# Kernel optimization log

Hardware: AMD Instinct MI355X
Metric: run time of the kernel (lower is better)

The kernel has to match this reference:

```python
import jax, jax.numpy as jnp
import numpy as np


def setup_inputs() -> dict:
    key = jax.random.key(0)
    ks = jax.random.split(key, 8)
    B, Nq, Nk, D, H, Cv = 8, 4096, 4096, 2, 64, 64
    q = jax.random.normal(ks[0], (B, Nq, D), dtype=jnp.float32)
    k = jax.random.normal(ks[1], (B, Nk, D), dtype=jnp.float32)
    v = jax.random.normal(ks[2], (B, Nk, Cv), dtype=jnp.float32)
    # Linear params (torch nn.Linear layout: W is (out, in), y = x @ W.T + b)
    s = 1.0 / np.sqrt(D)
    q_proj_w = jax.random.uniform(ks[3], (H, D), jnp.float32, -s, s)
    q_proj_b = jax.random.uniform(ks[4], (H,), jnp.float32, -s, s)
    k_proj_w = jax.random.uniform(ks[5], (H, D), jnp.float32, -s, s)
    k_proj_b = jax.random.uniform(ks[6], (H,), jnp.float32, -s, s)
    return {"q": q, "k": k, "v": v,
            "q_proj_w": q_proj_w, "q_proj_b": q_proj_b,
            "k_proj_w": k_proj_w, "k_proj_b": k_proj_b,
            "top_k": 16}


def _cdist(q, k):
    # Euclidean distances (B, Nq, Nk) via the Gram trick (avoids a BxNqxNkxD diff tensor)
    q2 = jnp.sum(q * q, axis=-1)  # (B, Nq)
    k2 = jnp.sum(k * k, axis=-1)  # (B, Nk)
    d2 = q2[:, :, None] + k2[:, None, :] - 2.0 * jnp.einsum('bqd,bnd->bqn', q, k)
    return jnp.sqrt(jnp.maximum(d2, 0.0))


def _batched_gather(inputs, idx):
    # inputs: (B, Nk, C), idx: (B, Nq, K) -> (B, Nq, K, C)
    return jax.vmap(lambda inp, ix: inp[ix])(inputs, idx)


def reference(q, k, v, q_proj_w, q_proj_b, k_proj_w, k_proj_b, top_k):
    dists = _cdist(q, k)                                   # (B, Nq, Nk)
    _, knn_idx = jax.lax.top_k(-dists, top_k)              # smallest distances
    k_knn = _batched_gather(k, knn_idx)                    # (B, Nq, K, D)
    v_knn = _batched_gather(v, knn_idx)                    # (B, Nq, K, Cv)
    q_emb = q @ q_proj_w.T + q_proj_b                      # (B, Nq, H)
    k_emb = k_knn @ k_proj_w.T + k_proj_b                  # (B, Nq, K, H)
    attn_scores = jnp.einsum('bqh,bqkh->bqk', q_emb, k_emb)
    attn = jax.nn.softmax(attn_scores, axis=-1)
    out = jnp.einsum('bqk,bqkc->bqc', attn, v_knn)         # (B, Nq, Cv)
    return out
```

## Files before the change

kernel.cpp:

```cpp
#include <hip/hip_runtime.h>
#include <stdint.h>

typedef uint64_t u64;
typedef uint32_t u32;

#define NB    8
#define NQ    4096
#define NKEY  4096
#define CV    64
#define KSEL  16
#define NWAVE 8
#define BLK   (NWAVE * 64)
#define CMAX  64

#define PADV ((((u64)0x7F800000u) << 32) | (u64)0xFFFFFFFFu)

__device__ __forceinline__ u64 shflxor_u64(u64 v, int m) {
    const u32 lo = __shfl_xor((int)(u32)v, m);
    const u32 hi = __shfl_xor((int)(u32)(v >> 32), m);
    return (((u64)hi) << 32) | lo;
}

__device__ __forceinline__ float lanesort64_f32(float v, int lane) {
#pragma unroll
    for (int k = 2; k <= 64; k <<= 1) {
#pragma unroll
        for (int j = k >> 1; j > 0; j >>= 1) {
            const float p = __shfl_xor(v, j);
            const bool up    = ((lane & k) == 0);
            const bool lower = ((lane & j) == 0);
            v = (lower == up) ? fminf(v, p) : fmaxf(v, p);
        }
    }
    return v;
}

__device__ __forceinline__ u64 lanesort64_u64(u64 v, int lane) {
#pragma unroll
    for (int k = 2; k <= 64; k <<= 1) {
#pragma unroll
        for (int j = k >> 1; j > 0; j >>= 1) {
            const u64 p = shflxor_u64(v, j);
            const bool up    = ((lane & k) == 0);
            const bool lower = ((lane & j) == 0);
            const u64 mn = v < p ? v : p;
            const u64 mx = v < p ? p : v;
            v = (lower == up) ? mn : mx;
        }
    }
    return v;
}

extern "C" __global__ void setup_sums_kernel(const float* __restrict__ qw,
                                             const float* __restrict__ qb,
                                             const float* __restrict__ kw,
                                             const float* __restrict__ kb,
                                             float* __restrict__ w9) {
    const int h = threadIdx.x & 63;
    const float2 a = ((const float2*)qw)[h];
    const float2 c = ((const float2*)kw)[h];
    const float qbh = qb[h], kbh = kb[h];
    float s[9] = { a.x * c.x, a.y * c.x, qbh * c.x,
                   a.x * c.y, a.y * c.y, qbh * c.y,
                   a.x * kbh, a.y * kbh, qbh * kbh };
#pragma unroll
    for (int i = 0; i < 9; ++i)
#pragma unroll
        for (int off = 32; off; off >>= 1) s[i] += __shfl_xor(s[i], off);
    if (h == 0) {
#pragma unroll
        for (int i = 0; i < 9; ++i) w9[i] = s[i];
    }
}

extern "C" __global__ void __launch_bounds__(BLK, 2)
sparse_bev_attn_kernel(const float* __restrict__ qg,
                       const float* __restrict__ kg,
                       const float* __restrict__ vg,
                       const float* __restrict__ sums9,
                       float* __restrict__ outg)
{
    __shared__ u64 cand[NWAVE][CMAX];

    const int tid  = threadIdx.x;
    const int wv   = tid >> 6;
    const int lane = tid & 63;
    const int b    = blockIdx.x >> 9;
    const int qi   = ((blockIdx.x & 511) << 3) + wv;

    const float2* kp = (const float2*)(kg + (size_t)b * NKEY * 2);
    const float2  qc = ((const float2*)qg)[(size_t)b * NQ + qi];
    const float qx = qc.x, qy = qc.y;

    const float4* kp4 = (const float4*)kp;
    float d2r[64];
    float mn = __builtin_inff();
#pragma unroll
    for (int c = 0; c < 32; ++c) {
        const float4 kk = kp4[c * 64 + lane];
        const float dx0 = qx - kk.x, dy0 = qy - kk.y;
        const float dx1 = qx - kk.z, dy1 = qy - kk.w;
        d2r[2 * c]     = fmaf(dx0, dx0, dy0 * dy0);
        d2r[2 * c + 1] = fmaf(dx1, dx1, dy1 * dy1);
        mn = fminf(mn, fminf(d2r[2 * c], d2r[2 * c + 1]));
    }

    const float thr = __shfl(lanesort64_f32(mn, lane), 15);

    const u32 l2 = (u32)(lane << 1);
    auto collect = [&](float t) -> int {
        int c = 0;
#pragma unroll
        for (int r = 0; r < 64; ++r) {
            const bool acc = d2r[r] <= t;
            const u64 mask = __ballot(acc);
            if (mask) {
                const int pos = c + (int)__builtin_amdgcn_mbcnt_hi(
                    (u32)(mask >> 32), __builtin_amdgcn_mbcnt_lo((u32)mask, 0));
                if (acc && pos < CMAX) {
                    const u32 kidx = (u32)(((r >> 1) << 7) + (r & 1)) + l2;
                    cand[wv][pos] = (((u64)__float_as_uint(d2r[r])) << 32) | kidx;
                }
                c += __popcll(mask);
            }
        }
        return c;
    };

    int cnt = collect(thr);
    if (cnt > CMAX) {
        u32 lo = 0, hi = 0x7F800000u;
        while (lo < hi) {
            const u32 mid = (lo + hi) >> 1;
            const float t = __uint_as_float(mid);
            int c = 0;
#pragma unroll
            for (int r = 0; r < 64; ++r) c += (d2r[r] <= t) ? 1 : 0;
#pragma unroll
            for (int off = 32; off; off >>= 1) c += __shfl_xor(c, off);
            if (c >= KSEL) hi = mid; else lo = mid + 1;
        }
        cnt = collect(__uint_as_float(lo));
        if (cnt > CMAX) cnt = CMAX;
    }

    u64 myv = (lane < cnt) ? cand[wv][lane] : PADV;
    myv = lanesort64_u64(myv, lane);
    const u32 myidx = (u32)myv;

    const float s1 = sums9[0], s2 = sums9[1], s3 = sums9[2];
    const float s4 = sums9[3], s5 = sums9[4], s6 = sums9[5];
    const float s7 = sums9[6], s8 = sums9[7], s9 = sums9[8];
    const float A  = fmaf(qx, s1, fmaf(qy, s2, s3));
    const float Bb = fmaf(qx, s4, fmaf(qy, s5, s6));
    const float Cc = fmaf(qx, s7, fmaf(qy, s8, s9));

    const int sel = (lane < KSEL) ? (int)myidx : 0;
    const float2 kc = kp[sel];
    const float score = fmaf(A, kc.x, fmaf(Bb, kc.y, Cc));
    float mx = score;
#pragma unroll
    for (int off = 8; off; off >>= 1) mx = fmaxf(mx, __shfl_xor(mx, off));
    const float e = __expf(score - mx);
    float sum = e;
#pragma unroll
    for (int off = 8; off; off >>= 1) sum += __shfl_xor(sum, off);
    const float w = e / sum;

    const float* vb = vg + (size_t)b * NKEY * CV;
    float acc = 0.f;
#pragma unroll
    for (int s = 0; s < KSEL; ++s) {
        const u32 id   = (u32)__builtin_amdgcn_readlane((int)myidx, s);
        const float ws = __uint_as_float(
            (u32)__builtin_amdgcn_readlane((int)__float_as_uint(w), s));
        acc = fmaf(ws, vb[(size_t)id * CV + lane], acc);
    }
    outg[((size_t)b * NQ + qi) * CV + lane] = acc;
}

extern "C" void kernel_launch(void* const* d_in, const int* in_sizes, int n_in,
                              void* d_out, int out_size, void* d_ws, size_t ws_size,
                              hipStream_t stream) {
    const float* q  = (const float*)d_in[0];
    const float* k  = (const float*)d_in[1];
    const float* v  = (const float*)d_in[2];
    const float* qw = (const float*)d_in[3];
    const float* qb = (const float*)d_in[4];
    const float* kw = (const float*)d_in[5];
    const float* kb = (const float*)d_in[6];
    float* out = (float*)d_out;
    float* w9  = (float*)d_ws;

    hipLaunchKernelGGL(setup_sums_kernel, dim3(1), dim3(64), 0, stream,
                       qw, qb, kw, kb, w9);
    hipLaunchKernelGGL(sparse_bev_attn_kernel, dim3(NB * (NQ / NWAVE)), dim3(BLK),
                       0, stream, q, k, v, w9, out);
}
```

Baseline: 74.94 us.

## Recompute distances in two passes instead of caching 64 per lane

Drops the 64-register distance array. Distances are now recomputed in a min pass and again in a collect pass, which lowers register pressure and raises the launch-bounds occupancy target, with the block size halved to 4 waves. When workspace allows, a setup pass precomputes per-key (x, y, |k|^2) so each distance becomes two FMAs in Gram form. The full 64-lane bitonic sort is replaced by a partial top-16 network. The cost is a second read of all keys per query, and the Gram form may change near-tie ordering.

```diff
diff --git a/kernel.cpp b/kernel.cpp
--- a/kernel.cpp
+++ b/kernel.cpp
@@ -9,16 +9,23 @@
 #define NKEY  4096
 #define CV    64
 #define KSEL  16
-#define NWAVE 8
+#define NWAVE 4
 #define BLK   (NWAVE * 64)
 #define CMAX  64
-
-#define PADV ((((u64)0x7F800000u) << 32) | (u64)0xFFFFFFFFu)
+#define PADU  (~(u64)0)
 
 __device__ __forceinline__ u64 shflxor_u64(u64 v, int m) {
     const u32 lo = __shfl_xor((int)(u32)v, m);
     const u32 hi = __shfl_xor((int)(u32)(v >> 32), m);
     return (((u64)hi) << 32) | lo;
+}
+__device__ __forceinline__ int mbcnt64(u64 m) {
+    return (int)__builtin_amdgcn_mbcnt_hi((u32)(m >> 32),
+               __builtin_amdgcn_mbcnt_lo((u32)m, 0));
+}
+__device__ __forceinline__ u32 fkey(float f) {
+    const u32 b = __float_as_uint(f);
+    return b ^ (0x80000000u | (u32)((int32_t)b >> 31));
 }
 
 __device__ __forceinline__ float lanesort64_f32(float v, int lane) {
@@ -35,125 +42,208 @@
     return v;
 }
 
-__device__ __forceinline__ u64 lanesort64_u64(u64 v, int lane) {
-#pragma unroll
-    for (int k = 2; k <= 64; k <<= 1) {
+__device__ __forceinline__ u64 top16of64(u64 v, int lane) {
+#pragma unroll
+    for (int k = 2; k <= 16; k <<= 1) {
 #pragma unroll
         for (int j = k >> 1; j > 0; j >>= 1) {
             const u64 p = shflxor_u64(v, j);
             const bool up    = ((lane & k) == 0);
             const bool lower = ((lane & j) == 0);
-            const u64 mn = v < p ? v : p;
-            const u64 mx = v < p ? p : v;
+            const u64 mn = v < p ? v : p, mx = v < p ? p : v;
             v = (lower == up) ? mn : mx;
         }
     }
+    {   const u64 p = shflxor_u64(v, 16);
+        const u64 mn = v < p ? v : p, mx = v < p ? p : v;
+        v = ((lane & 16) == 0) ? mn : mx; }
+#pragma unroll
+    for (int j = 8; j > 0; j >>= 1) {
+        const u64 p = shflxor_u64(v, j);
+        const bool lower = ((lane & j) == 0);
+        const bool dasc  = ((lane & 32) == 0);
+        const u64 mn = v < p ? v : p, mx = v < p ? p : v;
+        v = (lower == dasc) ? mn : mx;
+    }
+    {   const u64 p = shflxor_u64(v, 32);
+        const u64 mn = v < p ? v : p, mx = v < p ? p : v;
+        v = ((lane & 32) == 0) ? mn : mx; }
     return v;
 }
 
-extern "C" __global__ void setup_sums_kernel(const float* __restrict__ qw,
-                                             const float* __restrict__ qb,
-                                             const float* __restrict__ kw,
-                                             const float* __restrict__ kb,
-                                             float* __restrict__ w9) {
-    const int h = threadIdx.x & 63;
-    const float2 a = ((const float2*)qw)[h];
-    const float2 c = ((const float2*)kw)[h];
-    const float qbh = qb[h], kbh = kb[h];
-    float s[9] = { a.x * c.x, a.y * c.x, qbh * c.x,
-                   a.x * c.y, a.y * c.y, qbh * c.y,
-                   a.x * kbh, a.y * kbh, qbh * kbh };
-#pragma unroll
-    for (int i = 0; i < 9; ++i)
-#pragma unroll
-        for (int off = 32; off; off >>= 1) s[i] += __shfl_xor(s[i], off);
-    if (h == 0) {
-#pragma unroll
-        for (int i = 0; i < 9; ++i) w9[i] = s[i];
-    }
-}
-
-extern "C" __global__ void __launch_bounds__(BLK, 2)
-sparse_bev_attn_kernel(const float* __restrict__ qg,
-                       const float* __restrict__ kg,
-                       const float* __restrict__ vg,
-                       const float* __restrict__ sums9,
-                       float* __restrict__ outg)
+__global__ void setup_kernel(const float* __restrict__ kg,
+                             const float* __restrict__ qw, const float* __restrict__ qb,
+                             const float* __restrict__ kw, const float* __restrict__ kb,
+                             float* __restrict__ w9, float4* __restrict__ kq4, int dok2)
+{
+    const int gid = blockIdx.x * 256 + threadIdx.x;
+    if (dok2 && gid < NB * NKEY) {
+        const float2 kc = ((const float2*)kg)[gid];
+        kq4[gid] = make_float4(kc.x, kc.y, fmaf(kc.x, kc.x, kc.y * kc.y), 0.f);
+    }
+    if (blockIdx.x == 0 && threadIdx.x < 64) {
+        const int h = threadIdx.x;
+        const float2 a = ((const float2*)qw)[h];
+        const float2 c = ((const float2*)kw)[h];
+        const float qbh = qb[h], kbh = kb[h];
+        float s[9] = { a.x * c.x, a.y * c.x, qbh * c.x,
+                       a.x * c.y, a.y * c.y, qbh * c.y,
+                       a.x * kbh, a.y * kbh, qbh * kbh };
+#pragma unroll
+        for (int i = 0; i < 9; ++i)
+#pragma unroll
+            for (int off = 32; off; off >>= 1) s[i] += __shfl_xor(s[i], off);
+        if (h == 0) {
+#pragma unroll
+            for (int i = 0; i < 9; ++i) w9[i] = s[i];
+        }
+    }
+}
+
+template<int MODE>
+__global__ __launch_bounds__(BLK, 8) void bev_main(
+    const float* __restrict__ qg, const float* __restrict__ kg,
+    const float* __restrict__ vg, const float* __restrict__ w9,
+    const float4* __restrict__ kq4, float* __restrict__ outg)
 {
     __shared__ u64 cand[NWAVE][CMAX];
 
     const int tid  = threadIdx.x;
     const int wv   = tid >> 6;
     const int lane = tid & 63;
-    const int b    = blockIdx.x >> 9;
-    const int qi   = ((blockIdx.x & 511) << 3) + wv;
+    const int b    = blockIdx.x >> 10;
+    const int qi   = ((blockIdx.x & 1023) << 2) + wv;
 
     const float2* kp = (const float2*)(kg + (size_t)b * NKEY * 2);
     const float2  qc = ((const float2*)qg)[(size_t)b * NQ + qi];
     const float qx = qc.x, qy = qc.y;
-
+    const float m2qx = -2.f * qx, m2qy = -2.f * qy;
+    const float4* kb4 = kq4 + (size_t)b * NKEY;
     const float4* kp4 = (const float4*)kp;
-    float d2r[64];
-    float mn = __builtin_inff();
-#pragma unroll
-    for (int c = 0; c < 32; ++c) {
-        const float4 kk = kp4[c * 64 + lane];
-        const float dx0 = qx - kk.x, dy0 = qy - kk.y;
-        const float dx1 = qx - kk.z, dy1 = qy - kk.w;
-        d2r[2 * c]     = fmaf(dx0, dx0, dy0 * dy0);
-        d2r[2 * c + 1] = fmaf(dx1, dx1, dy1 * dy1);
-        mn = fminf(mn, fminf(d2r[2 * c], d2r[2 * c + 1]));
-    }
-
+
+    float mn0 = __builtin_inff(), mn1 = mn0, mn2 = mn0, mn3 = mn0;
+    if (MODE == 0) {
+#pragma unroll
+        for (int c = 0; c < 64; c += 4) {
+            const float4 a0 = kb4[(c + 0) * 64 + lane];
+            const float4 a1 = kb4[(c + 1) * 64 + lane];
+            const float4 a2 = kb4[(c + 2) * 64 + lane];
+            const float4 a3 = kb4[(c + 3) * 64 + lane];
+            mn0 = fminf(mn0, fmaf(a0.x, m2qx, fmaf(a0.y, m2qy, a0.z)));
+            mn1 = fminf(mn1, fmaf(a1.x, m2qx, fmaf(a1.y, m2qy, a1.z)));
+            mn2 = fminf(mn2, fmaf(a2.x, m2qx, fmaf(a2.y, m2qy, a2.z)));
+            mn3 = fminf(mn3, fmaf(a3.x, m2qx, fmaf(a3.y, m2qy, a3.z)));
+        }
+    } else {
+#pragma unroll
+        for (int c = 0; c < 32; c += 2) {
+            const float4 k0 = kp4[(c + 0) * 64 + lane];
+            const float4 k1 = kp4[(c + 1) * 64 + lane];
+            { const float dx = qx - k0.x, dy = qy - k0.y; mn0 = fminf(mn0, fmaf(dx, dx, dy * dy)); }
+            { const float dx = qx - k0.z, dy = qy - k0.w; mn1 = fminf(mn1, fmaf(dx, dx, dy * dy)); }
+            { const float dx = qx - k1.x, dy = qy - k1.y; mn2 = fminf(mn2, fmaf(dx, dx, dy * dy)); }
+            { const float dx = qx - k1.z, dy = qy - k1.w; mn3 = fminf(mn3, fmaf(dx, dx, dy * dy)); }
+        }
+    }
+    const float mn  = fminf(fminf(mn0, mn1), fminf(mn2, mn3));
     const float thr = __shfl(lanesort64_f32(mn, lane), 15);
 
-    const u32 l2 = (u32)(lane << 1);
-    auto collect = [&](float t) -> int {
-        int c = 0;
-#pragma unroll
-        for (int r = 0; r < 64; ++r) {
-            const bool acc = d2r[r] <= t;
-            const u64 mask = __ballot(acc);
-            if (mask) {
-                const int pos = c + (int)__builtin_amdgcn_mbcnt_hi(
-                    (u32)(mask >> 32), __builtin_amdgcn_mbcnt_lo((u32)mask, 0));
-                if (acc && pos < CMAX) {
-                    const u32 kidx = (u32)(((r >> 1) << 7) + (r & 1)) + l2;
-                    cand[wv][pos] = (((u64)__float_as_uint(d2r[r])) << 32) | kidx;
+    int cnt = 0;
+    if (MODE == 0) {
+#pragma unroll
+        for (int c = 0; c < 64; ++c) {
+            const float4 a = kb4[c * 64 + lane];
+            const float vv = fmaf(a.x, m2qx, fmaf(a.y, m2qy, a.z));
+            const bool acc = vv <= thr;
+            const u64 mk = __ballot(acc);
+            if (mk) {
+                const int pos = cnt + mbcnt64(mk);
+                if (acc && pos < CMAX)
+                    cand[wv][pos] = (((u64)fkey(vv)) << 32) | (u32)(c * 64 + lane);
+                cnt += __popcll(mk);
+            }
+        }
+    } else {
+#pragma unroll
+        for (int c = 0; c < 32; ++c) {
+            const float4 kk = kp4[c * 64 + lane];
+            const float dx0 = qx - kk.x, dy0 = qy - kk.y;
+            const float dx1 = qx - kk.z, dy1 = qy - kk.w;
+            const float v0 = fmaf(dx0, dx0, dy0 * dy0);
+            const float v1 = fmaf(dx1, dx1, dy1 * dy1);
+            const bool a0 = v0 <= thr;
+            u64 mk = __ballot(a0);
+            if (mk) {
+                const int pos = cnt + mbcnt64(mk);
+                if (a0 && pos < CMAX)
+                    cand[wv][pos] = (((u64)fkey(v0)) << 32) | (u32)(2 * (c * 64 + lane));
+                cnt += __popcll(mk);
+            }
+            const bool a1 = v1 <= thr;
+            mk = __ballot(a1);
+            if (mk) {
+                const int pos = cnt + mbcnt64(mk);
+                if (a1 && pos < CMAX)
+                    cand[wv][pos] = (((u64)fkey(v1)) << 32) | (u32)(2 * (c * 64 + lane) + 1);
+                cnt += __popcll(mk);
+            }
+        }
+    }
+
+    if (cnt > CMAX) {
+        u32 lo = 0, hi = ~0u;
+        while (lo < hi) {
+            const u32 mid = lo + ((hi - lo) >> 1);
+            int cc = 0;
+#pragma unroll 1
+            for (int c = 0; c < 64; ++c) {
+                float vv;
+                if (MODE == 0) {
+                    const float4 a = kb4[c * 64 + lane];
+                    vv = fmaf(a.x, m2qx, fmaf(a.y, m2qy, a.z));
+                } else {
+                    const float2 kc2 = kp[c * 64 + lane];
+                    const float dx = qx - kc2.x, dy = qy - kc2.y;
+                    vv = fmaf(dx, dx, dy * dy);
                 }
-                c += __popcll(mask);
-            }
-        }
-        return c;
-    };
-
-    int cnt = collect(thr);
-    if (cnt > CMAX) {
-        u32 lo = 0, hi = 0x7F800000u;
-        while (lo < hi) {
-            const u32 mid = (lo + hi) >> 1;
-            const float t = __uint_as_float(mid);
-            int c = 0;
-#pragma unroll
-            for (int r = 0; r < 64; ++r) c += (d2r[r] <= t) ? 1 : 0;
-#pragma unroll
-            for (int off = 32; off; off >>= 1) c += __shfl_xor(c, off);
-            if (c >= KSEL) hi = mid; else lo = mid + 1;
-        }
-        cnt = collect(__uint_as_float(lo));
+                cc += (fkey(vv) <= mid) ? 1 : 0;
+            }
+#pragma unroll
+            for (int off = 32; off; off >>= 1) cc += __shfl_xor(cc, off);
+            if (cc >= KSEL) hi = mid; else lo = mid + 1;
+        }
+        cnt = 0;
+#pragma unroll 1
+        for (int c = 0; c < 64; ++c) {
+            float vv;
+            if (MODE == 0) {
+                const float4 a = kb4[c * 64 + lane];
+                vv = fmaf(a.x, m2qx, fmaf(a.y, m2qy, a.z));
+            } else {
+                const float2 kc2 = kp[c * 64 + lane];
+                const float dx = qx - kc2.x, dy = qy - kc2.y;
+                vv = fmaf(dx, dx, dy * dy);
+            }
+            const u32 tb = fkey(vv);
+            const bool acc = tb <= lo;
+            const u64 mk = __ballot(acc);
+            if (mk) {
+                const int pos = cnt + mbcnt64(mk);
+                if (acc && pos < CMAX)
+                    cand[wv][pos] = (((u64)tb) << 32) | (u32)(c * 64 + lane);
+                cnt += __popcll(mk);
+            }
+        }
         if (cnt > CMAX) cnt = CMAX;
     }
 
-    u64 myv = (lane < cnt) ? cand[wv][lane] : PADV;
-    myv = lanesort64_u64(myv, lane);
+    u64 myv = (lane < cnt) ? cand[wv][lane] : PADU;
+    myv = top16of64(myv, lane);
     const u32 myidx = (u32)myv;
 
-    const float s1 = sums9[0], s2 = sums9[1], s3 = sums9[2];
-    const float s4 = sums9[3], s5 = sums9[4], s6 = sums9[5];
-    const float s7 = sums9[6], s8 = sums9[7], s9 = sums9[8];
-    const float A  = fmaf(qx, s1, fmaf(qy, s2, s3));
-    const float Bb = fmaf(qx, s4, fmaf(qy, s5, s6));
-    const float Cc = fmaf(qx, s7, fmaf(qy, s8, s9));
+    const float A  = fmaf(qx, w9[0], fmaf(qy, w9[1], w9[2]));
+    const float Bb = fmaf(qx, w9[3], fmaf(qy, w9[4], w9[5]));
+    const float Cc = fmaf(qx, w9[6], fmaf(qy, w9[7], w9[8]));
 
     const int sel = (lane < KSEL) ? (int)myidx : 0;
     const float2 kc = kp[sel];
@@ -190,10 +280,18 @@
     const float* kw = (const float*)d_in[5];
     const float* kb = (const float*)d_in[6];
     float* out = (float*)d_out;
-    float* w9  = (float*)d_ws;
-
-    hipLaunchKernelGGL(setup_sums_kernel, dim3(1), dim3(64), 0, stream,
-                       qw, qb, kw, kb, w9);
-    hipLaunchKernelGGL(sparse_bev_attn_kernel, dim3(NB * (NQ / NWAVE)), dim3(BLK),
-                       0, stream, q, k, v, w9, out);
-}
+
+    float*  w9  = (float*)d_ws;
+    float4* kq4 = (float4*)((char*)d_ws + 256);
+    const size_t need = 256 + (size_t)NB * NKEY * sizeof(float4);
+    const int mode0 = (ws_size >= need) ? 1 : 0;
+
+    hipLaunchKernelGGL(setup_kernel, dim3(mode0 ? (NB * NKEY / 256) : 1), dim3(256),
+                       0, stream, k, qw, qb, kw, kb, w9, kq4, mode0);
+    if (mode0)
+        hipLaunchKernelGGL((bev_main<0>), dim3(NB * NQ / NWAVE), dim3(BLK),
+                           0, stream, q, k, v, w9, kq4, out);
+    else
+        hipLaunchKernelGGL((bev_main<1>), dim3(NB * NQ / NWAVE), dim3(BLK),
+                           0, stream, q, k, v, w9, kq4, out);
+}
```

Measured after the change: 186.7 us. +149.1%, slower.

## Process eight queries per wave with two-pass recompute and partial top-16 sort

Applied to the files above, without the earlier changes.

Each wave now handles eight queries, so every key load is shared across them. Instead of keeping 64 distances in registers, the kernel runs a min pass, then recomputes distances in a collect pass using the expanded form k² − 2q·k, and uses an order-preserving float key. The full 64-lane bitonic sort is replaced by a partial network that only needs the top 16, and occupancy hints and block size change. The cost is recomputing distances and more per-wave serial work; the expanded form can change which neighbour wins near ties.

```diff
diff --git a/kernel.cpp b/kernel.cpp
--- a/kernel.cpp
+++ b/kernel.cpp
@@ -9,16 +9,24 @@
 #define NKEY  4096
 #define CV    64
 #define KSEL  16
-#define NWAVE 8
+#define G     8
+#define NWAVE 4
 #define BLK   (NWAVE * 64)
 #define CMAX  64
-
-#define PADV ((((u64)0x7F800000u) << 32) | (u64)0xFFFFFFFFu)
+#define PADU  (~(u64)0)
 
 __device__ __forceinline__ u64 shflxor_u64(u64 v, int m) {
     const u32 lo = __shfl_xor((int)(u32)v, m);
     const u32 hi = __shfl_xor((int)(u32)(v >> 32), m);
     return (((u64)hi) << 32) | lo;
+}
+__device__ __forceinline__ int mbcnt64(u64 m) {
+    return (int)__builtin_amdgcn_mbcnt_hi((u32)(m >> 32),
+               __builtin_amdgcn_mbcnt_lo((u32)m, 0));
+}
+__device__ __forceinline__ u32 fkey(float f) {
+    const u32 b = __float_as_uint(f);
+    return b ^ (0x80000000u | (u32)((int32_t)b >> 31));
 }
 
 __device__ __forceinline__ float lanesort64_f32(float v, int lane) {
@@ -35,27 +43,39 @@
     return v;
 }
 
-__device__ __forceinline__ u64 lanesort64_u64(u64 v, int lane) {
-#pragma unroll
-    for (int k = 2; k <= 64; k <<= 1) {
+__device__ __forceinline__ u64 top16of64(u64 v, int lane) {
+#pragma unroll
+    for (int k = 2; k <= 16; k <<= 1) {
 #pragma unroll
         for (int j = k >> 1; j > 0; j >>= 1) {
             const u64 p = shflxor_u64(v, j);
             const bool up    = ((lane & k) == 0);
             const bool lower = ((lane & j) == 0);
-            const u64 mn = v < p ? v : p;
-            const u64 mx = v < p ? p : v;
+            const u64 mn = v < p ? v : p, mx = v < p ? p : v;
             v = (lower == up) ? mn : mx;
         }
     }
+    {   const u64 p = shflxor_u64(v, 16);
+        const u64 mn = v < p ? v : p, mx = v < p ? p : v;
+        v = ((lane & 16) == 0) ? mn : mx; }
+#pragma unroll
+    for (int j = 8; j > 0; j >>= 1) {
+        const u64 p = shflxor_u64(v, j);
+        const bool lower = ((lane & j) == 0);
+        const bool dasc  = ((lane & 32) == 0);
+        const u64 mn = v < p ? v : p, mx = v < p ? p : v;
+        v = (lower == dasc) ? mn : mx;
+    }
+    {   const u64 p = shflxor_u64(v, 32);
+        const u64 mn = v < p ? v : p, mx = v < p ? p : v;
+        v = ((lane & 32) == 0) ? mn : mx; }
     return v;
 }
 
-extern "C" __global__ void setup_sums_kernel(const float* __restrict__ qw,
-                                             const float* __restrict__ qb,
-                                             const float* __restrict__ kw,
-                                             const float* __restrict__ kb,
-                                             float* __restrict__ w9) {
+__global__ void setup_kernel(const float* __restrict__ qw, const float* __restrict__ qb,
+                             const float* __restrict__ kw, const float* __restrict__ kb,
+                             float* __restrict__ w9)
+{
     const int h = threadIdx.x & 63;
     const float2 a = ((const float2*)qw)[h];
     const float2 c = ((const float2*)kw)[h];
@@ -73,110 +93,165 @@
     }
 }
 
-extern "C" __global__ void __launch_bounds__(BLK, 2)
-sparse_bev_attn_kernel(const float* __restrict__ qg,
-                       const float* __restrict__ kg,
-                       const float* __restrict__ vg,
-                       const float* __restrict__ sums9,
-                       float* __restrict__ outg)
+extern "C" __global__ __launch_bounds__(BLK, 4) void bev_main(
+    const float* __restrict__ qg, const float* __restrict__ kg,
+    const float* __restrict__ vg, const float* __restrict__ w9,
+    float* __restrict__ outg)
 {
-    __shared__ u64 cand[NWAVE][CMAX];
+    __shared__ u64 cand[NWAVE][G][CMAX];
 
     const int tid  = threadIdx.x;
     const int wv   = tid >> 6;
     const int lane = tid & 63;
-    const int b    = blockIdx.x >> 9;
-    const int qi   = ((blockIdx.x & 511) << 3) + wv;
-
-    const float2* kp = (const float2*)(kg + (size_t)b * NKEY * 2);
-    const float2  qc = ((const float2*)qg)[(size_t)b * NQ + qi];
-    const float qx = qc.x, qy = qc.y;
-
+    const int wvu  = __builtin_amdgcn_readfirstlane(wv);
+    const int b    = blockIdx.x >> 7;
+    const int qbase = ((int)(blockIdx.x & 127) * NWAVE + wvu) * G;
+
+    const float2* kp  = (const float2*)(kg + (size_t)b * NKEY * 2);
     const float4* kp4 = (const float4*)kp;
-    float d2r[64];
-    float mn = __builtin_inff();
-#pragma unroll
+    const float2* qp  = (const float2*)qg + (size_t)b * NQ + qbase;
+
+    float qxx[G], qyy[G], m2x[G], m2y[G];
+#pragma unroll
+    for (int q = 0; q < G; ++q) {
+        const float2 qc = qp[q];
+        qxx[q] = qc.x; qyy[q] = qc.y;
+        m2x[q] = -2.f * qc.x; m2y[q] = -2.f * qc.y;
+    }
+
+    float mn[G];
+#pragma unroll
+    for (int q = 0; q < G; ++q) mn[q] = __builtin_inff();
+#pragma unroll 8
     for (int c = 0; c < 32; ++c) {
         const float4 kk = kp4[c * 64 + lane];
-        const float dx0 = qx - kk.x, dy0 = qy - kk.y;
-        const float dx1 = qx - kk.z, dy1 = qy - kk.w;
-        d2r[2 * c]     = fmaf(dx0, dx0, dy0 * dy0);
-        d2r[2 * c + 1] = fmaf(dx1, dx1, dy1 * dy1);
-        mn = fminf(mn, fminf(d2r[2 * c], d2r[2 * c + 1]));
-    }
-
-    const float thr = __shfl(lanesort64_f32(mn, lane), 15);
-
-    const u32 l2 = (u32)(lane << 1);
-    auto collect = [&](float t) -> int {
-        int c = 0;
-#pragma unroll
-        for (int r = 0; r < 64; ++r) {
-            const bool acc = d2r[r] <= t;
-            const u64 mask = __ballot(acc);
-            if (mask) {
-                const int pos = c + (int)__builtin_amdgcn_mbcnt_hi(
-                    (u32)(mask >> 32), __builtin_amdgcn_mbcnt_lo((u32)mask, 0));
-                if (acc && pos < CMAX) {
-                    const u32 kidx = (u32)(((r >> 1) << 7) + (r & 1)) + l2;
-                    cand[wv][pos] = (((u64)__float_as_uint(d2r[r])) << 32) | kidx;
+        const float k2a = fmaf(kk.x, kk.x, kk.y * kk.y);
+        const float k2b = fmaf(kk.z, kk.z, kk.w * kk.w);
+#pragma unroll
+        for (int q = 0; q < G; ++q) {
+            const float va = fmaf(kk.x, m2x[q], fmaf(kk.y, m2y[q], k2a));
+            const float vb = fmaf(kk.z, m2x[q], fmaf(kk.w, m2y[q], k2b));
+            mn[q] = fminf(mn[q], fminf(va, vb));
+        }
+    }
+
+    float thr[G];
+#pragma unroll
+    for (int q = 0; q < G; ++q)
+        thr[q] = __shfl(lanesort64_f32(mn[q], lane), 15);
+
+    int cnt[G];
+#pragma unroll
+    for (int q = 0; q < G; ++q) cnt[q] = 0;
+#pragma unroll 4
+    for (int c = 0; c < 32; ++c) {
+        const float4 kk = kp4[c * 64 + lane];
+        const float k2a = fmaf(kk.x, kk.x, kk.y * kk.y);
+        const float k2b = fmaf(kk.z, kk.z, kk.w * kk.w);
+        const u32 ia = (u32)(2 * (c * 64 + lane));
+#pragma unroll
+        for (int q = 0; q < G; ++q) {
+            const float va = fmaf(kk.x, m2x[q], fmaf(kk.y, m2y[q], k2a));
+            const float vb = fmaf(kk.z, m2x[q], fmaf(kk.w, m2y[q], k2b));
+            const bool aa = va <= thr[q];
+            const bool ab = vb <= thr[q];
+            const u64 mka = __ballot(aa);
+            const u64 mkb = __ballot(ab);
+            if (mka | mkb) {
+                const int posa = cnt[q] + mbcnt64(mka);
+                cnt[q] += (int)__popcll(mka);
+                const int posb = cnt[q] + mbcnt64(mkb);
+                cnt[q] += (int)__popcll(mkb);
+                if (aa && posa < CMAX)
+                    cand[wv][q][posa] = (((u64)fkey(va)) << 32) | ia;
+                if (ab && posb < CMAX)
+                    cand[wv][q][posb] = (((u64)fkey(vb)) << 32) | (ia + 1);
+            }
+        }
+    }
+
+#pragma unroll
+    for (int q = 0; q < G; ++q) {
+        if (cnt[q] > CMAX) {
+            u32 lo = 0, hi = ~0u;
+            while (lo < hi) {
+                const u32 mid = lo + ((hi - lo) >> 1);
+                int cc = 0;
+#pragma unroll 1
+                for (int c = 0; c < 32; ++c) {
+                    const float4 kk = kp4[c * 64 + lane];
+                    const float k2a = fmaf(kk.x, kk.x, kk.y * kk.y);
+                    const float k2b = fmaf(kk.z, kk.z, kk.w * kk.w);
+                    const float va = fmaf(kk.x, m2x[q], fmaf(kk.y, m2y[q], k2a));
+                    const float vb = fmaf(kk.z, m2x[q], fmaf(kk.w, m2y[q], k2b));
+                    cc += (fkey(va) <= mid) ? 1 : 0;
+                    cc += (fkey(vb) <= mid) ? 1 : 0;
                 }
-                c += __popcll(mask);
+#pragma unroll
+                for (int off = 32; off; off >>= 1) cc += __shfl_xor(cc, off);
+                if (cc >= KSEL) hi = mid; else lo = mid + 1;
             }
-        }
-        return c;
-    };
-
-    int cnt = collect(thr);
-    if (cnt > CMAX) {
-        u32 lo = 0, hi = 0x7F800000u;
-        while (lo < hi) {
-            const u32 mid = (lo + hi) >> 1;
-            const float t = __uint_as_float(mid);
-            int c = 0;
-#pragma unroll
-            for (int r = 0; r < 64; ++r) c += (d2r[r] <= t) ? 1 : 0;
-#pragma unroll
-            for (int off = 32; off; off >>= 1) c += __shfl_xor(c, off);
-            if (c >= KSEL) hi = mid; else lo = mid + 1;
-        }
-        cnt = collect(__uint_as_float(lo));
-        if (cnt > CMAX) cnt = CMAX;
-    }
-
-    u64 myv = (lane < cnt) ? cand[wv][lane] : PADV;
-    myv = lanesort64_u64(myv, lane);
-    const u32 myidx = (u32)myv;
-
-    const float s1 = sums9[0], s2 = sums9[1], s3 = sums9[2];
-    const float s4 = sums9[3], s5 = sums9[4], s6 = sums9[5];
-    const float s7 = sums9[6], s8 = sums9[7], s9 = sums9[8];
-    const float A  = fmaf(qx, s1, fmaf(qy, s2, s3));
-    const float Bb = fmaf(qx, s4, fmaf(qy, s5, s6));
-    const float Cc = fmaf(qx, s7, fmaf(qy, s8, s9));
-
-    const int sel = (lane < KSEL) ? (int)myidx : 0;
-    const float2 kc = kp[sel];
-    const float score = fmaf(A, kc.x, fmaf(Bb, kc.y, Cc));
-    float mx = score;
-#pragma unroll
-    for (int off = 8; off; off >>= 1) mx = fmaxf(mx, __shfl_xor(mx, off));
-    const float e = __expf(score - mx);
-    float sum = e;
-#pragma unroll
-    for (int off = 8; off; off >>= 1) sum += __shfl_xor(sum, off);
-    const float w = e / sum;
-
+            int cc = 0;
+#pragma unroll 1
+            for (int c = 0; c < 32; ++c) {
+                const float4 kk = kp4[c * 64 + lane];
+                const float k2a = fmaf(kk.x, kk.x, kk.y * kk.y);
+                const float k2b = fmaf(kk.z, kk.z, kk.w * kk.w);
+                const float va = fmaf(kk.x, m2x[q], fmaf(kk.y, m2y[q], k2a));
+                const float vb = fmaf(kk.z, m2x[q], fmaf(kk.w, m2y[q], k2b));
+                const u32 ta = fkey(va), tb = fkey(vb);
+                const bool aa = ta <= lo, ab = tb <= lo;
+                const u64 mka = __ballot(aa);
+                const u64 mkb = __ballot(ab);
+                const int posa = cc + mbcnt64(mka);
+                cc += (int)__popcll(mka);
+                const int posb = cc + mbcnt64(mkb);
+                cc += (int)__popcll(mkb);
+                const u32 ia = (u32)(2 * (c * 64 + lane));
+                if (aa && posa < CMAX) cand[wv][q][posa] = (((u64)ta) << 32) | ia;
+                if (ab && posb < CMAX) cand[wv][q][posb] = (((u64)tb) << 32) | (ia + 1);
+            }
+            cnt[q] = cc < CMAX ? cc : CMAX;
+        }
+    }
+
+    const float s1 = w9[0], s2 = w9[1], s3 = w9[2];
+    const float s4 = w9[3], s5 = w9[4], s6 = w9[5];
+    const float s7 = w9[6], s8 = w9[7], s9 = w9[8];
     const float* vb = vg + (size_t)b * NKEY * CV;
-    float acc = 0.f;
-#pragma unroll
-    for (int s = 0; s < KSEL; ++s) {
-        const u32 id   = (u32)__builtin_amdgcn_readlane((int)myidx, s);
-        const float ws = __uint_as_float(
-            (u32)__builtin_amdgcn_readlane((int)__float_as_uint(w), s));
-        acc = fmaf(ws, vb[(size_t)id * CV + lane], acc);
-    }
-    outg[((size_t)b * NQ + qi) * CV + lane] = acc;
+
+#pragma unroll 1
+    for (int q = 0; q < G; ++q) {
+        u64 myv = (lane < cnt[q]) ? cand[wv][q][lane] : PADU;
+        myv = top16of64(myv, lane);
+        const u32 myidx = (u32)myv;
+
+        const float A  = fmaf(qxx[q], s1, fmaf(qyy[q], s2, s3));
+        const float Bb = fmaf(qxx[q], s4, fmaf(qyy[q], s5, s6));
+        const float Cc = fmaf(qxx[q], s7, fmaf(qyy[q], s8, s9));
+
+        const int sel = (lane < KSEL) ? (int)myidx : 0;
+        const float2 kc = kp[sel];
+        const float score = fmaf(A, kc.x, fmaf(Bb, kc.y, Cc));
+        float mx = score;
+#pragma unroll
+        for (int off = 8; off; off >>= 1) mx = fmaxf(mx, __shfl_xor(mx, off));
+        const float e = __expf(score - mx);
+        float sum = e;
+#pragma unroll
+        for (int off = 8; off; off >>= 1) sum += __shfl_xor(sum, off);
+        const float w = e / sum;
+
+        float acc = 0.f;
+#pragma unroll
+        for (int s = 0; s < KSEL; ++s) {
+            const u32 id   = (u32)__builtin_amdgcn_readlane((int)myidx, s);
+            const float ws = __uint_as_float(
+                (u32)__builtin_amdgcn_readlane((int)__float_as_uint(w), s));
+            acc = fmaf(ws, vb[(size_t)id * CV + lane], acc);
+        }
+        outg[((size_t)b * NQ + qbase + q) * CV + lane] = acc;
+    }
 }
 
 extern "C" void kernel_launch(void* const* d_in, const int* in_sizes, int n_in,
@@ -192,8 +267,8 @@
     float* out = (float*)d_out;
     float* w9  = (float*)d_ws;
 
-    hipLaunchKernelGGL(setup_sums_kernel, dim3(1), dim3(64), 0, stream,
+    hipLaunchKernelGGL(setup_kernel, dim3(1), dim3(64), 0, stream,
                        qw, qb, kw, kb, w9);
-    hipLaunchKernelGGL(sparse_bev_attn_kernel, dim3(NB * (NQ / NWAVE)), dim3(BLK),
+    hipLaunchKernelGGL(bev_main, dim3(NB * NQ / (G * NWAVE)), dim3(BLK),
                        0, stream, q, k, v, w9, out);
 }
```

After: 74.86 us. About the same (-0.1%).

## Replace brute-force kNN scan with uniform spatial grid search

Applied to the files above, without the earlier changes.

Keys are bucketed into a 64x64 uniform grid per batch by count, scan and scatter kernels, so each query only examines keys in nearby cells. The search grows a square window until enough candidates are found, takes a threshold from them, then visits outer rings of cells and prunes each cell by its box distance against the current 16th-best. This removes the full 4096-key distance scan per query at the cost of four extra small launches, atomics and data-dependent divergent loops. The grid spans the fixed range [-4,4] with clamping, so results stay exact but cost rises if keys are not spread out.

```diff
diff --git a/kernel.cpp b/kernel.cpp
--- a/kernel.cpp
+++ b/kernel.cpp
@@ -3,22 +3,37 @@
 
 typedef uint64_t u64;
 typedef uint32_t u32;
+typedef unsigned short u16;
 
 #define NB    8
 #define NQ    4096
 #define NKEY  4096
 #define CV    64
 #define KSEL  16
-#define NWAVE 8
-#define BLK   (NWAVE * 64)
-#define CMAX  64
-
-#define PADV ((((u64)0x7F800000u) << 32) | (u64)0xFFFFFFFFu)
+#define GRD   64
+#define NCELL (GRD * GRD)
+#define HCELL 0.125f
+#define GLO   -4.0f
+#define CTGT  48
+#define CMAX  128
+#define PADU  (~(u64)0)
+
+#define WS_CS    256
+#define WS_SKEY  (WS_CS + NB * NCELL * 4)
+#define WS_SIDX  (WS_SKEY + NB * NKEY * 8)
 
 __device__ __forceinline__ u64 shflxor_u64(u64 v, int m) {
     const u32 lo = __shfl_xor((int)(u32)v, m);
     const u32 hi = __shfl_xor((int)(u32)(v >> 32), m);
     return (((u64)hi) << 32) | lo;
+}
+__device__ __forceinline__ int mbcnt64(u64 m) {
+    return (int)__builtin_amdgcn_mbcnt_hi((u32)(m >> 32),
+               __builtin_amdgcn_mbcnt_lo((u32)m, 0));
+}
+__device__ __forceinline__ int cellof(float x) {
+    int c = (int)floorf((x - GLO) * 8.0f);
+    return c < 0 ? 0 : (c > GRD - 1 ? GRD - 1 : c);
 }
 
 __device__ __forceinline__ float lanesort64_f32(float v, int lane) {
@@ -35,27 +50,74 @@
     return v;
 }
 
-__device__ __forceinline__ u64 lanesort64_u64(u64 v, int lane) {
-#pragma unroll
-    for (int k = 2; k <= 64; k <<= 1) {
+__device__ __forceinline__ u64 top16of64(u64 v, int lane) {
+#pragma unroll
+    for (int k = 2; k <= 16; k <<= 1) {
 #pragma unroll
         for (int j = k >> 1; j > 0; j >>= 1) {
             const u64 p = shflxor_u64(v, j);
             const bool up    = ((lane & k) == 0);
             const bool lower = ((lane & j) == 0);
-            const u64 mn = v < p ? v : p;
-            const u64 mx = v < p ? p : v;
+            const u64 mn = v < p ? v : p, mx = v < p ? p : v;
             v = (lower == up) ? mn : mx;
         }
     }
+    {   const u64 p = shflxor_u64(v, 16);
+        const u64 mn = v < p ? v : p, mx = v < p ? p : v;
+        v = ((lane & 16) == 0) ? mn : mx; }
+#pragma unroll
+    for (int j = 8; j > 0; j >>= 1) {
+        const u64 p = shflxor_u64(v, j);
+        const bool lower = ((lane & j) == 0);
+        const bool dasc  = ((lane & 32) == 0);
+        const u64 mn = v < p ? v : p, mx = v < p ? p : v;
+        v = (lower == dasc) ? mn : mx;
+    }
+    {   const u64 p = shflxor_u64(v, 32);
+        const u64 mn = v < p ? v : p, mx = v < p ? p : v;
+        v = ((lane & 32) == 0) ? mn : mx; }
     return v;
 }
 
-extern "C" __global__ void setup_sums_kernel(const float* __restrict__ qw,
-                                             const float* __restrict__ qb,
-                                             const float* __restrict__ kw,
-                                             const float* __restrict__ kb,
-                                             float* __restrict__ w9) {
+__global__ void k_zero(u32* __restrict__ cs) {
+    cs[blockIdx.x * 256 + threadIdx.x] = 0u;
+}
+__global__ void k_count(const float* __restrict__ kg, u32* __restrict__ cs) {
+    const int gid = blockIdx.x * 256 + threadIdx.x;
+    const float2 kk = ((const float2*)kg)[gid];
+    const int cell = cellof(kk.y) * GRD + cellof(kk.x);
+    atomicAdd(&cs[(gid >> 12) * NCELL + cell], 1u);
+}
+__global__ void k_scan(u32* __restrict__ cs) {
+    u32* c = cs + blockIdx.x * NCELL;
+    const int lane = threadIdx.x & 63;
+    u32 carry = 0;
+#pragma unroll 1
+    for (int i = 0; i < NCELL / 64; ++i) {
+        const u32 v = c[i * 64 + lane];
+        u32 s = v;
+#pragma unroll
+        for (int off = 1; off < 64; off <<= 1) {
+            const u32 t = __shfl_up(s, off);
+            if (lane >= off) s += t;
+        }
+        c[i * 64 + lane] = s - v + carry;
+        carry += (u32)__shfl(s, 63);
+    }
+}
+__global__ void k_scatter(const float* __restrict__ kg, u32* __restrict__ cs,
+                          float2* __restrict__ skey, u16* __restrict__ sidx) {
+    const int gid = blockIdx.x * 256 + threadIdx.x;
+    const float2 kk = ((const float2*)kg)[gid];
+    const int b = gid >> 12;
+    const int cell = cellof(kk.y) * GRD + cellof(kk.x);
+    const u32 p = atomicAdd(&cs[b * NCELL + cell], 1u);
+    skey[b * NKEY + p] = kk;
+    sidx[b * NKEY + p] = (u16)(gid & 4095);
+}
+__global__ void k_sums(const float* __restrict__ qw, const float* __restrict__ qb,
+                       const float* __restrict__ kw, const float* __restrict__ kb,
+                       float* __restrict__ w9) {
     const int h = threadIdx.x & 63;
     const float2 a = ((const float2*)qw)[h];
     const float2 c = ((const float2*)kw)[h];
@@ -73,88 +135,203 @@
     }
 }
 
-extern "C" __global__ void __launch_bounds__(BLK, 2)
-sparse_bev_attn_kernel(const float* __restrict__ qg,
-                       const float* __restrict__ kg,
-                       const float* __restrict__ vg,
-                       const float* __restrict__ sums9,
-                       float* __restrict__ outg)
+extern "C" __global__ __launch_bounds__(256, 8) void bev_grid(
+    const float* __restrict__ qg, const float* __restrict__ kg,
+    const float* __restrict__ vg, const float* __restrict__ w9,
+    const u32* __restrict__ cs_g, const float2* __restrict__ skey_g,
+    const u16* __restrict__ sidx_g, float* __restrict__ outg)
 {
-    __shared__ u64 cand[NWAVE][CMAX];
-
-    const int tid  = threadIdx.x;
-    const int wv   = tid >> 6;
-    const int lane = tid & 63;
-    const int b    = blockIdx.x >> 9;
-    const int qi   = ((blockIdx.x & 511) << 3) + wv;
-
-    const float2* kp = (const float2*)(kg + (size_t)b * NKEY * 2);
-    const float2  qc = ((const float2*)qg)[(size_t)b * NQ + qi];
+    __shared__ u64 cand[4][CMAX];
+
+    const int tid = threadIdx.x, wv = tid >> 6, lane = tid & 63;
+    const int gw = blockIdx.x * 4 + wv;
+    const int b  = gw >> 12;
+    const int qi = gw & 4095;
+
+    const float2 qc = ((const float2*)qg)[(size_t)b * NQ + qi];
     const float qx = qc.x, qy = qc.y;
-
-    const float4* kp4 = (const float4*)kp;
-    float d2r[64];
-    float mn = __builtin_inff();
-#pragma unroll
-    for (int c = 0; c < 32; ++c) {
-        const float4 kk = kp4[c * 64 + lane];
-        const float dx0 = qx - kk.x, dy0 = qy - kk.y;
-        const float dx1 = qx - kk.z, dy1 = qy - kk.w;
-        d2r[2 * c]     = fmaf(dx0, dx0, dy0 * dy0);
-        d2r[2 * c + 1] = fmaf(dx1, dx1, dy1 * dy1);
-        mn = fminf(mn, fminf(d2r[2 * c], d2r[2 * c + 1]));
-    }
-
-    const float thr = __shfl(lanesort64_f32(mn, lane), 15);
-
-    const u32 l2 = (u32)(lane << 1);
-    auto collect = [&](float t) -> int {
-        int c = 0;
-#pragma unroll
-        for (int r = 0; r < 64; ++r) {
-            const bool acc = d2r[r] <= t;
-            const u64 mask = __ballot(acc);
-            if (mask) {
-                const int pos = c + (int)__builtin_amdgcn_mbcnt_hi(
-                    (u32)(mask >> 32), __builtin_amdgcn_mbcnt_lo((u32)mask, 0));
-                if (acc && pos < CMAX) {
-                    const u32 kidx = (u32)(((r >> 1) << 7) + (r & 1)) + l2;
-                    cand[wv][pos] = (((u64)__float_as_uint(d2r[r])) << 32) | kidx;
+    const u32*    cs = cs_g   + b * NCELL;
+    const float2* sk = skey_g + b * NKEY;
+    const u16*    si = sidx_g + b * NKEY;
+    u64* cd = cand[wv];
+
+    const int qcx = __builtin_amdgcn_readfirstlane(cellof(qx));
+    const int qcy = __builtin_amdgcn_readfirstlane(cellof(qy));
+
+    int R = 1, cx0, cx1, ry0, ry1, L;
+#pragma unroll 1
+    for (;;) {
+        cx0 = qcx - R < 0 ? 0 : qcx - R;  cx1 = qcx + R > 63 ? 63 : qcx + R;
+        ry0 = qcy - R < 0 ? 0 : qcy - R;  ry1 = qcy + R > 63 ? 63 : qcy + R;
+        L = 0;
+#pragma unroll 1
+        for (int ry = ry0; ry <= ry1; ++ry) {
+            const int c0 = ry * GRD + cx0;
+            const int lo = c0 ? (int)cs[c0 - 1] : 0;
+            L += (int)cs[ry * GRD + cx1] - lo;
+        }
+        if (L >= CTGT || R >= 63) break;
+        ++R;
+    }
+
+    float mnv = __builtin_inff();
+    int cum = 0;
+#pragma unroll 1
+    for (int ry = ry0; ry <= ry1; ++ry) {
+        const int c0 = ry * GRD + cx0;
+        const int lo = c0 ? (int)cs[c0 - 1] : 0;
+        const int len = (int)cs[ry * GRD + cx1] - lo;
+        int off = 0;
+#pragma unroll 1
+        while (off < len) {
+            const int sl = cum & 63;
+            const int n  = (64 - sl) < (len - off) ? (64 - sl) : (len - off);
+            if (lane >= sl && lane < sl + n) {
+                const float2 kk = sk[lo + off + lane - sl];
+                const float dx = qx - kk.x, dy = qy - kk.y;
+                mnv = fminf(mnv, fmaf(dx, dx, dy * dy));
+            }
+            off += n; cum += n;
+        }
+    }
+    const float T = __shfl(lanesort64_f32(mnv, lane), 15);
+
+    int cnt = 0; cum = 0;
+#pragma unroll 1
+    for (int ry = ry0; ry <= ry1; ++ry) {
+        const int c0 = ry * GRD + cx0;
+        const int lo = c0 ? (int)cs[c0 - 1] : 0;
+        const int len = (int)cs[ry * GRD + cx1] - lo;
+        int off = 0;
+#pragma unroll 1
+        while (off < len) {
+            const int sl = cum & 63;
+            const int n  = (64 - sl) < (len - off) ? (64 - sl) : (len - off);
+            const bool act = (lane >= sl) && (lane < sl + n);
+            const int pos = lo + off + lane - sl;
+            float d2 = __builtin_inff();
+            if (act) {
+                const float2 kk = sk[pos];
+                const float dx = qx - kk.x, dy = qy - kk.y;
+                d2 = fmaf(dx, dx, dy * dy);
+            }
+            const bool acc = act && (d2 <= T);
+            const u64 mk = __ballot(acc);
+            if (mk) {
+                const int p = cnt + mbcnt64(mk);
+                if (acc && p < CMAX)
+                    cd[p] = (((u64)__float_as_uint(d2)) << 32) | (u32)si[pos];
+                cnt += (int)__popcll(mk);
+            }
+            off += n; cum += n;
+        }
+    }
+    if (cnt > CMAX) cnt = CMAX;
+
+    u64 myv = (lane < (cnt < 64 ? cnt : 64)) ? cd[lane] : PADU;
+    myv = top16of64(myv, lane);
+    {
+        int base = 64, rem = cnt - 64;
+#pragma unroll 1
+        while (rem > 0) {
+            const int take = rem < 48 ? rem : 48;
+            const u64 inv = (lane < 16) ? myv
+                          : ((lane - 16 < take) ? cd[base + lane - 16] : PADU);
+            myv = top16of64(inv, lane);
+            base += take; rem -= take;
+        }
+    }
+
+    u64 b16; float d16f;
+    {
+        u64 m = myv;
+#pragma unroll
+        for (int off = 8; off; off >>= 1) { const u64 p = shflxor_u64(m, off); m = p > m ? p : m; }
+        const u32 mlo = (u32)__builtin_amdgcn_readlane((int)(u32)m, 0);
+        const u32 mhi = (u32)__builtin_amdgcn_readlane((int)(u32)(m >> 32), 0);
+        b16 = (((u64)mhi) << 32) | mlo;
+        d16f = __uint_as_float(mhi);
+    }
+
+    int ecnt = 0;
+    {
+        auto refresh = [&]() {
+            u64 m = myv;
+#pragma unroll
+            for (int off = 8; off; off >>= 1) { const u64 p = shflxor_u64(m, off); m = p > m ? p : m; }
+            const u32 mlo = (u32)__builtin_amdgcn_readlane((int)(u32)m, 0);
+            const u32 mhi = (u32)__builtin_amdgcn_readlane((int)(u32)(m >> 32), 0);
+            b16 = (((u64)mhi) << 32) | mlo;
+            d16f = __uint_as_float(mhi);
+        };
+        auto flush = [&]() {
+#pragma unroll 1
+            while (ecnt > 0) {
+                const int take = ecnt < 48 ? ecnt : 48;
+                const u64 inv = (lane < 16) ? myv
+                              : ((lane - 16 < take) ? cd[ecnt - take + lane - 16] : PADU);
+                myv = top16of64(inv, lane);
+                ecnt -= take;
+            }
+            refresh();
+        };
+        auto doCell = [&](int cx, int cy) {
+            const float xlo = GLO + cx * HCELL, xhi = xlo + HCELL;
+            const float ylo = GLO + cy * HCELL, yhi = ylo + HCELL;
+            float dx = fmaxf((cx == 0) ? 0.f : (xlo - qx), (cx == GRD - 1) ? 0.f : (qx - xhi));
+            float dy = fmaxf((cy == 0) ? 0.f : (ylo - qy), (cy == GRD - 1) ? 0.f : (qy - yhi));
+            dx = fmaxf(dx, 0.f); dy = fmaxf(dy, 0.f);
+            if (fmaf(dx, dx, dy * dy) > d16f) return;
+            const int c = cy * GRD + cx;
+            const int lo = c ? (int)cs[c - 1] : 0;
+            const int len = (int)cs[c] - lo;
+#pragma unroll 1
+            for (int off = 0; off < len; off += 64) {
+                const bool act = lane < (len - off < 64 ? len - off : 64);
+                const int pos = lo + off + lane;
+                u64 pk = PADU;
+                if (act) {
+                    const float2 kk = sk[pos];
+                    const float ddx = qx - kk.x, ddy = qy - kk.y;
+                    const float d2 = fmaf(ddx, ddx, ddy * ddy);
+                    pk = (((u64)__float_as_uint(d2)) << 32) | (u32)si[pos];
                 }
-                c += __popcll(mask);
-            }
-        }
-        return c;
-    };
-
-    int cnt = collect(thr);
-    if (cnt > CMAX) {
-        u32 lo = 0, hi = 0x7F800000u;
-        while (lo < hi) {
-            const u32 mid = (lo + hi) >> 1;
-            const float t = __uint_as_float(mid);
-            int c = 0;
-#pragma unroll
-            for (int r = 0; r < 64; ++r) c += (d2r[r] <= t) ? 1 : 0;
-#pragma unroll
-            for (int off = 32; off; off >>= 1) c += __shfl_xor(c, off);
-            if (c >= KSEL) hi = mid; else lo = mid + 1;
-        }
-        cnt = collect(__uint_as_float(lo));
-        if (cnt > CMAX) cnt = CMAX;
-    }
-
-    u64 myv = (lane < cnt) ? cand[wv][lane] : PADV;
-    myv = lanesort64_u64(myv, lane);
+                const bool acc = act && (pk < b16);
+                const u64 mk = __ballot(acc);
+                if (mk) {
+                    const int p = ecnt + mbcnt64(mk);
+                    if (acc && p < CMAX) cd[p] = pk;
+                    ecnt += (int)__popcll(mk);
+                    if (ecnt > CMAX) ecnt = CMAX;
+                }
+            }
+            if (ecnt >= 48) flush();
+        };
+
+        int D = R + 1;
+#pragma unroll 1
+        for (;;) {
+            const float rb = (float)(D - 1) * HCELL;
+            if (rb * rb > d16f) break;
+            const int xa = qcx - D, xb = qcx + D, ya = qcy - D, yb = qcy + D;
+            if (xa < 0 && xb > 63 && ya < 0 && yb > 63) break;
+            const int cxa = xa < 0 ? 0 : xa, cxb = xb > 63 ? 63 : xb;
+            if (ya >= 0) for (int cx = cxa; cx <= cxb; ++cx) doCell(cx, ya);
+            if (yb <= 63) for (int cx = cxa; cx <= cxb; ++cx) doCell(cx, yb);
+            const int cya = (ya + 1) < 0 ? 0 : ya + 1, cyb = (yb - 1) > 63 ? 63 : yb - 1;
+            if (xa >= 0) for (int cy = cya; cy <= cyb; ++cy) doCell(xa, cy);
+            if (xb <= 63) for (int cy = cya; cy <= cyb; ++cy) doCell(xb, cy);
+            ++D;
+        }
+        if (ecnt > 0) flush();
+    }
+
     const u32 myidx = (u32)myv;
-
-    const float s1 = sums9[0], s2 = sums9[1], s3 = sums9[2];
-    const float s4 = sums9[3], s5 = sums9[4], s6 = sums9[5];
-    const float s7 = sums9[6], s8 = sums9[7], s9 = sums9[8];
-    const float A  = fmaf(qx, s1, fmaf(qy, s2, s3));
-    const float Bb = fmaf(qx, s4, fmaf(qy, s5, s6));
-    const float Cc = fmaf(qx, s7, fmaf(qy, s8, s9));
-
+    const float A  = fmaf(qx, w9[0], fmaf(qy, w9[1], w9[2]));
+    const float Bb = fmaf(qx, w9[3], fmaf(qy, w9[4], w9[5]));
+    const float Cc = fmaf(qx, w9[6], fmaf(qy, w9[7], w9[8]));
+
+    const float2* kp = (const float2*)kg + (size_t)b * NKEY;
     const int sel = (lane < KSEL) ? (int)myidx : 0;
     const float2 kc = kp[sel];
     const float score = fmaf(A, kc.x, fmaf(Bb, kc.y, Cc));
@@ -190,10 +367,17 @@
     const float* kw = (const float*)d_in[5];
     const float* kb = (const float*)d_in[6];
     float* out = (float*)d_out;
-    float* w9  = (float*)d_ws;
-
-    hipLaunchKernelGGL(setup_sums_kernel, dim3(1), dim3(64), 0, stream,
-                       qw, qb, kw, kb, w9);
-    hipLaunchKernelGGL(sparse_bev_attn_kernel, dim3(NB * (NQ / NWAVE)), dim3(BLK),
-                       0, stream, q, k, v, w9, out);
-}
+
+    float*  w9   = (float*)d_ws;
+    u32*    cs   = (u32*)((char*)d_ws + WS_CS);
+    float2* skey = (float2*)((char*)d_ws + WS_SKEY);
+    u16*    sidx = (u16*)((char*)d_ws + WS_SIDX);
+
+    hipLaunchKernelGGL(k_zero,    dim3(NB * NCELL / 256), dim3(256), 0, stream, cs);
+    hipLaunchKernelGGL(k_count,   dim3(NB * NKEY / 256),  dim3(256), 0, stream, k, cs);
+    hipLaunchKernelGGL(k_scan,    dim3(NB), dim3(64), 0, stream, cs);
+    hipLaunchKernelGGL(k_scatter, dim3(NB * NKEY / 256),  dim3(256), 0, stream, k, cs, skey, sidx);
+    hipLaunchKernelGGL(k_sums,    dim3(1), dim3(64), 0, stream, qw, qb, kw, kb, w9);
+    hipLaunchKernelGGL(bev_grid,  dim3(NB * NQ / 4), dim3(256), 0, stream,
+                       q, k, v, w9, cs, skey, sidx, out);
+}
```

After: 150.8 us. 2.01x slower.
